# Kernel tuning notes

Hardware: AMD Instinct MI355X
Metric: run time of the kernel (lower is better)

## Reference

```python
import jax, jax.numpy as jnp
import numpy as np

N, D, MAX_DEG, B = 100000, 256, 128, 1024
FANOUTS = (25, 10)
OUT = 128  # per-branch output dim; concat doubles it


def setup_inputs() -> dict:
    key = jax.random.key(0)
    ks = jax.random.split(key, 8)
    s1 = 1.0 / np.sqrt(D)
    return {
        "ids": jax.random.randint(ks[0], (B,), 0, N),
        "adj": jax.random.randint(ks[1], (N, MAX_DEG), 0, N),
        "feats": jax.random.normal(ks[2], (N, D), dtype=jnp.float32),
        "W1x": jax.random.normal(ks[3], (OUT, D), dtype=jnp.float32) * s1,
        "b1x": jnp.zeros((OUT,), jnp.float32),
        "W1n": jax.random.normal(ks[4], (OUT, D), dtype=jnp.float32) * s1,
        "b1n": jnp.zeros((OUT,), jnp.float32),
        "W2x": jax.random.normal(ks[5], (OUT, 2 * OUT), dtype=jnp.float32) * s1,
        "b2x": jnp.zeros((OUT,), jnp.float32),
        "W2n": jax.random.normal(ks[6], (OUT, 2 * OUT), dtype=jnp.float32) * s1,
        "b2n": jnp.zeros((OUT,), jnp.float32),
    }


def _sample(adj, ids, n_samples, key):
    # uniform_neib_sampler: one shared random column permutation, take first n
    perm = jax.random.permutation(key, adj.shape[1])
    return adj[ids][:, perm[:n_samples]].reshape(-1)  # flattened neighbor ids


def _agg(x, neibs, Wx, bx, Wn, bn, act):
    # MeanAggregator: concat(fc_x(x), fc_neib(mean over neighbors))
    m = neibs.reshape(x.shape[0], -1, neibs.shape[-1]).mean(axis=1)
    out = jnp.concatenate([x @ Wx.T + bx, m @ Wn.T + bn], axis=-1)
    return act(out) if act is not None else out


def reference(ids, adj, feats, W1x, b1x, W1n, b1n, W2x, b2x, W2n, b2n):
    k1, k2 = jax.random.split(jax.random.key(42))
    ids1 = _sample(adj, ids, FANOUTS[0], k1)      # [B*25]
    ids2 = _sample(adj, ids1, FANOUTS[1], k2)     # [B*25*10]
    h = [feats[ids], feats[ids1], feats[ids2]]    # gathers: the memory-bound core
    # layer 1 (relu) applied to each consecutive (self, neighbor) pair
    h = [_agg(h[k], h[k + 1], W1x, b1x, W1n, b1n, jax.nn.relu) for k in range(2)]
    # layer 2 (no activation)
    h = [_agg(h[0], h[1], W2x, b2x, W2n, b2n, None)]
    return h[0]  # [B, 256]
```

## Files before the change

### kernel.cpp

```cpp
#include <hip/hip_runtime.h>
#include <stdint.h>
#include <stddef.h>
#include <algorithm>


#define D       256
#define D4      64
#define BATCH   1024
#define F1      25
#define F2      10
#define MAXDEG  128
#define OUTD    128
#define SP      264
#define ZP      260

struct Perms { int p1[F1]; int p2[F2]; };

static inline uint32_t rotl32(uint32_t x, int d){ return (x<<d)|(x>>(32-d)); }

static void tf2x32(uint32_t k0, uint32_t k1, uint32_t x0, uint32_t x1,
                   uint32_t* o0, uint32_t* o1){
  uint32_t ks0=k0, ks1=k1, ks2 = k0^k1^0x1BD11BDAu;
  static const int rot[2][4] = {{13,15,26,6},{17,29,16,24}};
  x0 += ks0; x1 += ks1;
  for (int g=0; g<5; ++g){
    const int* r = rot[g&1];
    for (int i=0;i<4;++i){ x0 += x1; x1 = rotl32(x1, r[i]) ^ x0; }
    switch(g){
      case 0: x0 += ks1; x1 += ks2 + 1u; break;
      case 1: x0 += ks2; x1 += ks0 + 2u; break;
      case 2: x0 += ks0; x1 += ks1 + 3u; break;
      case 3: x0 += ks1; x1 += ks2 + 4u; break;
      default:x0 += ks2; x1 += ks0 + 5u; break;
    }
  }
  *o0 = x0; *o1 = x1;
}

static void mkperm(uint32_t ka, uint32_t kb, int n, int* outp){
  uint32_t ska, skb;
  tf2x32(ka, kb, 0u, 1u, &ska, &skb);
  uint32_t bits[MAXDEG];
  int idxs[MAXDEG];
  for (int i=0;i<MAXDEG;++i){
    uint32_t y0,y1; tf2x32(ska,skb, 0u,(uint32_t)i, &y0,&y1);
    bits[i] = y0 ^ y1;
    idxs[i] = i;
  }
  std::stable_sort(idxs, idxs+MAXDEG,
                   [&](int a,int b){ return bits[a] < bits[b]; });
  for (int j=0;j<n;++j) outp[j] = idxs[j];
}

static void compute_perms(Perms& P){
  uint32_t k1a,k1b,k2a,k2b;
  tf2x32(0u,42u, 0u,0u, &k1a,&k1b);
  tf2x32(0u,42u, 0u,1u, &k2a,&k2b);
  mkperm(k1a,k1b, F1, P.p1);
  mkperm(k2a,k2b, F2, P.p2);
}

typedef short s16x8 __attribute__((ext_vector_type(8)));
typedef float f32x4 __attribute__((ext_vector_type(4)));

__device__ __forceinline__ uint16_t f2bf(float f){
  uint32_t u = __float_as_uint(f);
  u += 0x7fffu + ((u >> 16) & 1u);
  return (uint16_t)(u >> 16);
}
__device__ __forceinline__ float bf2f(uint16_t h){
  return __uint_as_float(((uint32_t)h) << 16);
}

__global__ __launch_bounds__(256) void pack_k(
    const float* __restrict__ W1x, const float* __restrict__ W1n,
    const float* __restrict__ W2x, const float* __restrict__ W2n,
    uint16_t* __restrict__ WB, float* __restrict__ W2T){
  int g = blockIdx.x*256 + threadIdx.x;
  if (g < 8192){
    int kt = g >> 10, ct = (g >> 6) & 15, lane = g & 63;
    int n = ct*16 + (lane & 15);
    int k = kt*32 + (lane >> 4)*8;
    const float* src = (n < OUTD) ? (W1x + (size_t)n*D + k)
                                  : (W1n + (size_t)(n-OUTD)*D + k);
    float4 f0 = *(const float4*)src;
    float4 f1 = *(const float4*)(src + 4);
    uint32_t p[4] = {
      (uint32_t)f2bf(f0.x) | ((uint32_t)f2bf(f0.y)<<16),
      (uint32_t)f2bf(f0.z) | ((uint32_t)f2bf(f0.w)<<16),
      (uint32_t)f2bf(f1.x) | ((uint32_t)f2bf(f1.y)<<16),
      (uint32_t)f2bf(f1.z) | ((uint32_t)f2bf(f1.w)<<16) };
    *(uint4*)(WB + (size_t)g*8) = *(uint4*)p;
  } else {
    int idx = g - 8192;
    int k = idx >> 8, o = idx & 255;
    W2T[idx] = (o < OUTD) ? W2x[(size_t)o*D + k]
                          : W2n[(size_t)(o-OUTD)*D + k];
  }
}

#define ISSUE(Varr, j) \
  { const int* np_ = &nidx[(j)*F2]; \
    _Pragma("unroll") \
    for (int u=0;u<F2;++u) Varr[u] = feats4[(size_t)np_[u]*D4 + lane]; }

#define REDUCE_STORE(Varr, j) \
  { float4 s_ = Varr[0]; \
    _Pragma("unroll") \
    for (int u=1;u<F2;++u){ s_.x+=Varr[u].x; s_.y+=Varr[u].y; \
                            s_.z+=Varr[u].z; s_.w+=Varr[u].w; } \
    const float inv_ = 1.f/F2; \
    uint32_t p_[2] = { \
      (uint32_t)f2bf(s_.x*inv_) | ((uint32_t)f2bf(s_.y*inv_)<<16), \
      (uint32_t)f2bf(s_.z*inv_) | ((uint32_t)f2bf(s_.w*inv_)<<16) }; \
    *(uint2*)(S + (26+(j))*SP + lane*4) = *(uint2*)p_; }

__global__ __launch_bounds__(256, 4) void mega9_k(
    const float4* __restrict__ feats4,
    const int* __restrict__ ids, const int* __restrict__ adj,
    const uint16_t* __restrict__ WB, const float* __restrict__ W2T,
    const float* __restrict__ b1x, const float* __restrict__ b1n,
    const float* __restrict__ b2x, const float* __restrict__ b2n,
    float* __restrict__ out, Perms P)
{
  __shared__ uint16_t S[64*SP];
  __shared__ float    M2s[D];
  __shared__ float    Z0s[D];
  __shared__ int      sids[26];
  __shared__ int      nidx[F1*F2];

  const int b    = blockIdx.x;
  const int tid  = threadIdx.x;
  const int lane = tid & 63;
  const int w    = tid >> 6;
  const int ln   = lane & 15;
  const int q    = lane >> 4;
  const int id   = ids[b];
  uint16_t* Z = S;

  if (tid < F1) sids[tid] = adj[(size_t)id*MAXDEG + P.p1[tid]];
  if (tid == F1) sids[F1] = id;
  __syncthreads();
  if (tid < F1*F2){
    int j = tid / F2, u = tid - (tid/F2)*F2;
    nidx[tid] = adj[(size_t)sids[j]*MAXDEG + P.p2[u]];
  }
  __syncthreads();

  float4 va[7];
  #pragma unroll
  for (int l=0;l<7;++l){
    int idx = tid + l*256;
    if (idx < 26*D4)
      va[l] = feats4[(size_t)sids[idx>>6]*D4 + (idx&63)];
  }

  {
    float4 vA[F2], vB[F2];
    ISSUE(vA, w + 0);
    ISSUE(vB, w + 4);   REDUCE_STORE(vA, w + 0);
    ISSUE(vA, w + 8);   REDUCE_STORE(vB, w + 4);
    ISSUE(vB, w + 12);  REDUCE_STORE(vA, w + 8);
    ISSUE(vA, w + 16);  REDUCE_STORE(vB, w + 12);
    ISSUE(vB, w + 20);  REDUCE_STORE(vA, w + 16);
    if (w == 0){ ISSUE(vA, 24); }
    REDUCE_STORE(vB, w + 20);
    if (w == 0){ REDUCE_STORE(vA, 24); }
  }

  #pragma unroll
  for (int l=0;l<7;++l){
    int idx = tid + l*256;
    if (idx < 26*D4){
      int r = idx>>6, c4 = idx&63;
      uint32_t p[2] = { (uint32_t)f2bf(va[l].x) | ((uint32_t)f2bf(va[l].y)<<16),
                        (uint32_t)f2bf(va[l].z) | ((uint32_t)f2bf(va[l].w)<<16) };
      *(uint2*)(S + r*SP + c4*4) = *(uint2*)p;
    }
  }
  __syncthreads();

  {
    float s = 0.f;
    #pragma unroll
    for (int r=0;r<F1;++r) s += bf2f(S[r*SP + tid]);
    S[51*SP + tid] = f2bf(s * (1.f/F1));
  }
  __syncthreads();

  f32x4 acc[4][4];
  #pragma unroll
  for (int mt=0;mt<4;++mt)
    #pragma unroll
    for (int nt=0;nt<4;++nt) acc[mt][nt] = (f32x4){0.f,0.f,0.f,0.f};

  #pragma unroll 2
  for (int kt = 0; kt < 8; ++kt){
    s16x8 af[4], bfk[4];
    #pragma unroll
    for (int mt=0;mt<4;++mt)
      af[mt] = *(const s16x8*)(S + (mt*16 + ln)*SP + kt*32 + q*8);
    #pragma unroll
    for (int nt=0;nt<4;++nt)
      bfk[nt] = *(const s16x8*)(WB + (size_t)((kt*16 + w*4 + nt)*64 + lane)*8);
    #pragma unroll
    for (int mt=0;mt<4;++mt)
      #pragma unroll
      for (int nt=0;nt<4;++nt)
        acc[mt][nt] = __builtin_amdgcn_mfma_f32_16x16x32_bf16(
                        af[mt], bfk[nt], acc[mt][nt], 0, 0, 0);
  }
  __syncthreads();

  {
    const bool left = (w < 2);
    float bia[4];
    #pragma unroll
    for (int nt=0;nt<4;++nt){
      int n = w*64 + nt*16 + ln;
      bia[nt] = left ? b1x[n] : b1n[n-OUTD];
    }
    #pragma unroll
    for (int mt=0;mt<4;++mt)
      #pragma unroll
      for (int nt=0;nt<4;++nt){
        int n = w*64 + nt*16 + ln;
        #pragma unroll
        for (int reg=0;reg<4;++reg){
          int m = mt*16 + q*4 + reg;
          float val = fmaxf(acc[mt][nt][reg] + bia[nt], 0.f);
          if (left){
            if (m < 26) Z[m*ZP + n] = f2bf(val);
            if (m == 25) Z0s[n] = val;
          } else {
            if (m >= 26 && m < 52) Z[(m-26)*ZP + n] = f2bf(val);
            if (m == 51) Z0s[n] = val;
          }
        }
      }
  }
  __syncthreads();

  {
    float s = 0.f;
    #pragma unroll
    for (int r=0;r<F1;++r) s += bf2f(Z[r*ZP + tid]);
    M2s[tid] = s * (1.f/F1);
  }
  __syncthreads();

  {
    const int o = tid;
    const float* zsrc = (o < OUTD) ? Z0s : M2s;
    float a0=0.f, a1=0.f, a2=0.f, a3=0.f;
    #pragma unroll 8
    for (int k4=0;k4<D4;++k4){
      float4 z = *(const float4*)(zsrc + k4*4);
      const float* wp = W2T + (size_t)k4*4*D + o;
      a0 += z.x * wp[0];
      a1 += z.y * wp[D];
      a2 += z.z * wp[2*D];
      a3 += z.w * wp[3*D];
    }
    float acc2 = (a0 + a2) + (a1 + a3);
    acc2 += (o < OUTD) ? b2x[o] : b2n[o-OUTD];
    out[(size_t)b*D + o] = acc2;
  }
}

extern "C" void kernel_launch(void* const* d_in, const int* in_sizes, int n_in,
                              void* d_out, int out_size, void* d_ws, size_t ws_size,
                              hipStream_t stream){
  const int*   ids   = (const int*)  d_in[0];
  const int*   adj   = (const int*)  d_in[1];
  const float* feats = (const float*)d_in[2];
  const float* W1x   = (const float*)d_in[3];
  const float* b1x   = (const float*)d_in[4];
  const float* W1n   = (const float*)d_in[5];
  const float* b1n   = (const float*)d_in[6];
  const float* W2x   = (const float*)d_in[7];
  const float* b2x   = (const float*)d_in[8];
  const float* W2n   = (const float*)d_in[9];
  const float* b2n   = (const float*)d_in[10];
  float* out = (float*)d_out;

  Perms P;
  compute_perms(P);

  char* wsb = (char*)d_ws;
  uint16_t* WB  = (uint16_t*)wsb;
  wsb += (size_t)8192*8*sizeof(uint16_t);
  float*    W2T = (float*)wsb;

  hipLaunchKernelGGL(pack_k, dim3(288), dim3(256), 0, stream,
                     W1x, W1n, W2x, W2n, WB, W2T);
  hipLaunchKernelGGL(mega9_k, dim3(BATCH), dim3(256), 0, stream,
                     (const float4*)feats, ids, adj, WB, W2T,
                     b1x, b1n, b2x, b2n, out, P);
}
```

Measured before the change: 228.5 us.

## Double block size to 512 threads and split gathers and MFMA across eight waves

The fused GraphSAGE kernel now launches 512 threads per block instead of 256. The eight waves share the second-hop neighbour gathers, so each wave handles three groups instead of six. Self-row bf16 stores now overlap with the first neighbour gather. The layer-1 MFMA is split so each wave computes half the M tiles, which cuts accumulator registers. Extra threads sit idle during the per-column reductions and the layer-2 GEMV, and the higher launch bounds may constrain register allocation.

```diff
diff --git a/kernel.cpp b/kernel.cpp
--- a/kernel.cpp
+++ b/kernel.cpp
@@ -115,7 +115,7 @@
       (uint32_t)f2bf(s_.z*inv_) | ((uint32_t)f2bf(s_.w*inv_)<<16) }; \
     *(uint2*)(S + (26+(j))*SP + lane*4) = *(uint2*)p_; }
 
-__global__ __launch_bounds__(256, 4) void mega9_k(
+__global__ __launch_bounds__(512, 8) void mega11_k(
     const float4* __restrict__ feats4,
     const int* __restrict__ ids, const int* __restrict__ adj,
     const uint16_t* __restrict__ WB, const float* __restrict__ W2T,
@@ -147,40 +147,35 @@
   }
   __syncthreads();
 
-  float4 va[7];
-  #pragma unroll
-  for (int l=0;l<7;++l){
-    int idx = tid + l*256;
-    if (idx < 26*D4)
-      va[l] = feats4[(size_t)sids[idx>>6]*D4 + (idx&63)];
-  }
-
   {
+    float4 va[4];
+    #pragma unroll
+    for (int l=0;l<4;++l){
+      int idx = tid + l*512;
+      if (idx < 26*D4)
+        va[l] = feats4[(size_t)sids[idx>>6]*D4 + (idx&63)];
+    }
     float4 vA[F2], vB[F2];
-    ISSUE(vA, w + 0);
-    ISSUE(vB, w + 4);   REDUCE_STORE(vA, w + 0);
-    ISSUE(vA, w + 8);   REDUCE_STORE(vB, w + 4);
-    ISSUE(vB, w + 12);  REDUCE_STORE(vA, w + 8);
-    ISSUE(vA, w + 16);  REDUCE_STORE(vB, w + 12);
-    ISSUE(vB, w + 20);  REDUCE_STORE(vA, w + 16);
-    if (w == 0){ ISSUE(vA, 24); }
-    REDUCE_STORE(vB, w + 20);
-    if (w == 0){ REDUCE_STORE(vA, 24); }
-  }
-
-  #pragma unroll
-  for (int l=0;l<7;++l){
-    int idx = tid + l*256;
-    if (idx < 26*D4){
-      int r = idx>>6, c4 = idx&63;
-      uint32_t p[2] = { (uint32_t)f2bf(va[l].x) | ((uint32_t)f2bf(va[l].y)<<16),
-                        (uint32_t)f2bf(va[l].z) | ((uint32_t)f2bf(va[l].w)<<16) };
-      *(uint2*)(S + r*SP + c4*4) = *(uint2*)p;
-    }
-  }
-  __syncthreads();
-
-  {
+    ISSUE(vA, w);
+    #pragma unroll
+    for (int l=0;l<4;++l){
+      int idx = tid + l*512;
+      if (idx < 26*D4){
+        int r = idx>>6, c4 = idx&63;
+        uint32_t p[2] = { (uint32_t)f2bf(va[l].x) | ((uint32_t)f2bf(va[l].y)<<16),
+                          (uint32_t)f2bf(va[l].z) | ((uint32_t)f2bf(va[l].w)<<16) };
+        *(uint2*)(S + r*SP + c4*4) = *(uint2*)p;
+      }
+    }
+    ISSUE(vB, w + 8);   REDUCE_STORE(vA, w);
+    ISSUE(vA, w + 16);  REDUCE_STORE(vB, w + 8);
+    if (w == 0){ ISSUE(vB, 24); }
+    REDUCE_STORE(vA, w + 16);
+    if (w == 0){ REDUCE_STORE(vB, 24); }
+  }
+  __syncthreads();
+
+  if (tid < D){
     float s = 0.f;
     #pragma unroll
     for (int r=0;r<F1;++r) s += bf2f(S[r*SP + tid]);
@@ -188,47 +183,50 @@
   }
   __syncthreads();
 
-  f32x4 acc[4][4];
-  #pragma unroll
-  for (int mt=0;mt<4;++mt)
-    #pragma unroll
-    for (int nt=0;nt<4;++nt) acc[mt][nt] = (f32x4){0.f,0.f,0.f,0.f};
-
-  #pragma unroll 2
-  for (int kt = 0; kt < 8; ++kt){
-    s16x8 af[4], bfk[4];
-    #pragma unroll
-    for (int mt=0;mt<4;++mt)
-      af[mt] = *(const s16x8*)(S + (mt*16 + ln)*SP + kt*32 + q*8);
-    #pragma unroll
-    for (int nt=0;nt<4;++nt)
-      bfk[nt] = *(const s16x8*)(WB + (size_t)((kt*16 + w*4 + nt)*64 + lane)*8);
-    #pragma unroll
-    for (int mt=0;mt<4;++mt)
+  {
+    const int  wn   = w & 3;
+    const int  mh   = w >> 2;
+    const bool left = (wn < 2);
+    float bia[4];
+    #pragma unroll
+    for (int nt=0;nt<4;++nt){
+      int n = wn*64 + nt*16 + ln;
+      bia[nt] = left ? b1x[n] : b1n[n-OUTD];
+    }
+
+    f32x4 acc[2][4];
+    #pragma unroll
+    for (int mt2=0;mt2<2;++mt2)
+      #pragma unroll
+      for (int nt=0;nt<4;++nt) acc[mt2][nt] = (f32x4){0.f,0.f,0.f,0.f};
+
+    #pragma unroll 2
+    for (int kt = 0; kt < 8; ++kt){
+      s16x8 af[2], bfk[4];
+      #pragma unroll
+      for (int mt2=0;mt2<2;++mt2)
+        af[mt2] = *(const s16x8*)(S + ((mh*2+mt2)*16 + ln)*SP + kt*32 + q*8);
       #pragma unroll
       for (int nt=0;nt<4;++nt)
-        acc[mt][nt] = __builtin_amdgcn_mfma_f32_16x16x32_bf16(
-                        af[mt], bfk[nt], acc[mt][nt], 0, 0, 0);
-  }
-  __syncthreads();
-
-  {
-    const bool left = (w < 2);
-    float bia[4];
-    #pragma unroll
-    for (int nt=0;nt<4;++nt){
-      int n = w*64 + nt*16 + ln;
-      bia[nt] = left ? b1x[n] : b1n[n-OUTD];
-    }
-    #pragma unroll
-    for (int mt=0;mt<4;++mt)
+        bfk[nt] = *(const s16x8*)(WB + (size_t)((kt*16 + wn*4 + nt)*64 + lane)*8);
+      #pragma unroll
+      for (int mt2=0;mt2<2;++mt2)
+        #pragma unroll
+        for (int nt=0;nt<4;++nt)
+          acc[mt2][nt] = __builtin_amdgcn_mfma_f32_16x16x32_bf16(
+                           af[mt2], bfk[nt], acc[mt2][nt], 0, 0, 0);
+    }
+    __syncthreads();
+
+    #pragma unroll
+    for (int mt2=0;mt2<2;++mt2){
       #pragma unroll
       for (int nt=0;nt<4;++nt){
-        int n = w*64 + nt*16 + ln;
+        const int n = wn*64 + nt*16 + ln;
         #pragma unroll
         for (int reg=0;reg<4;++reg){
-          int m = mt*16 + q*4 + reg;
-          float val = fmaxf(acc[mt][nt][reg] + bia[nt], 0.f);
+          const int m = (mh*2+mt2)*16 + q*4 + reg;
+          float val = fmaxf(acc[mt2][nt][reg] + bia[nt], 0.f);
           if (left){
             if (m < 26) Z[m*ZP + n] = f2bf(val);
             if (m == 25) Z0s[n] = val;
@@ -238,10 +236,11 @@
           }
         }
       }
-  }
-  __syncthreads();
-
-  {
+    }
+  }
+  __syncthreads();
+
+  if (tid < D){
     float s = 0.f;
     #pragma unroll
     for (int r=0;r<F1;++r) s += bf2f(Z[r*ZP + tid]);
@@ -249,7 +248,7 @@
   }
   __syncthreads();
 
-  {
+  if (tid < D){
     const int o = tid;
     const float* zsrc = (o < OUTD) ? Z0s : M2s;
     float a0=0.f, a1=0.f, a2=0.f, a3=0.f;
@@ -294,7 +293,7 @@
 
   hipLaunchKernelGGL(pack_k, dim3(288), dim3(256), 0, stream,
                      W1x, W1n, W2x, W2n, WB, W2T);
-  hipLaunchKernelGGL(mega9_k, dim3(BATCH), dim3(256), 0, stream,
+  hipLaunchKernelGGL(mega11_k, dim3(BATCH), dim3(512), 0, stream,
                      (const float4*)feats, ids, adj, WB, W2T,
                      b1x, b1n, b2x, b2n, out, P);
 }
```

Result: slower. 267.1 us (+16.9%).
